# Performance work log

Hardware: AMD Instinct MI355X
Metric: run time of the kernel (lower is better)

Reference implementation:

```python
import jax, jax.numpy as jnp
import numpy as np

B, S, D, H = 4, 2048, 768, 12
DK = D // H

def setup_inputs() -> dict:
    key = jax.random.key(0)
    ks = jax.random.split(key, 9)
    s = 0.02
    return {
        "z": jax.random.normal(ks[0], (B, S, D), dtype=jnp.float32),
        "wq_w": jax.random.normal(ks[1], (D, D), dtype=jnp.float32) * s,
        "wq_b": jnp.zeros((D,), dtype=jnp.float32),
        "wk_w": jax.random.normal(ks[2], (D, D), dtype=jnp.float32) * s,
        "wk_b": jnp.zeros((D,), dtype=jnp.float32),
        "wv_w": jax.random.normal(ks[3], (D, D), dtype=jnp.float32) * s,
        "wv_b": jnp.zeros((D,), dtype=jnp.float32),
        "fc_w": jax.random.normal(ks[4], (D, D), dtype=jnp.float32) * s,
        "fc_b": jnp.zeros((D,), dtype=jnp.float32),
    }

def reference(z, wq_w, wq_b, wk_w, wk_b, wv_w, wv_b, fc_w, fc_b):
    # Dropout layers are treated as eval-mode (identity), as is standard for
    # a deterministic correctness baseline.
    b, s, d = z.shape
    temp = jnp.asarray(DK ** 0.5, dtype=z.dtype)
    # QKV projections -> [b, h, s, dk]
    def proj(w, bias):
        return (z @ w.T + bias).reshape(b, s, H, DK).transpose(0, 2, 1, 3)
    q = proj(wq_w, wq_b)
    k = proj(wk_w, wk_b)
    v = proj(wv_w, wv_b)
    # raw attention weights (pre-softmax), as returned by ScaleDotAttention
    attn_weights = jnp.einsum('bhqd,bhkd->bhqk', q / temp, k)  # [b,h,s,s]
    attn_probs = jax.nn.softmax(attn_weights, axis=-1)
    context = jnp.einsum('bhqk,bhkd->bhqd', attn_probs, v)  # [b,h,s,dk]
    avg_weights = jnp.sum(attn_weights, axis=1) / H  # [b,s,s]
    context = context.transpose(0, 2, 1, 3).reshape(b, s, d)
    attn_output = context @ fc_w.T + fc_b
    return attn_output, avg_weights
```

## Files before the change

### kernel.cpp

```cpp
#include <hip/hip_runtime.h>
#include <hip/hip_fp16.h>

#define Bc 4
#define Sc 2048
#define Dc 768
#define Hc 12
#define DKc 64

typedef _Float16 f16;
typedef __attribute__((ext_vector_type(8))) _Float16 f16x8;
typedef __attribute__((ext_vector_type(4))) _Float16 f16x4;
typedef __attribute__((ext_vector_type(4))) float f32x4;

static __device__ __forceinline__ f32x4 mfma16(f16x8 a, f16x8 b, f32x4 c) {
  return __builtin_amdgcn_mfma_f32_16x16x32_f16(a, b, c, 0, 0, 0);
}

#define GLD16(g, l)                                              \
  __builtin_amdgcn_global_load_lds(                              \
      (const __attribute__((address_space(1))) void*)(g),        \
      (__attribute__((address_space(3))) void*)(l), 16, 0, 0)

#define SWZ(row, colB) (((row) << 7) + ((colB) ^ (((row) & 7) << 4)))

__global__ __launch_bounds__(256) void cvt5(
    const float* __restrict__ z, const float* __restrict__ w0,
    const float* __restrict__ w1, const float* __restrict__ w2,
    const float* __restrict__ w3, f16* __restrict__ oz, f16* __restrict__ o0,
    f16* __restrict__ o1, f16* __restrict__ o2, f16* __restrict__ o3) {
  const int bid = blockIdx.x;
  const float* in;
  f16* out;
  int i0;
  if (bid < 6144)      { in = z;  out = oz; i0 = bid * 256; }
  else if (bid < 6720) { in = w0; out = o0; i0 = (bid - 6144) * 256; }
  else if (bid < 7296) { in = w1; out = o1; i0 = (bid - 6720) * 256; }
  else if (bid < 7872) { in = w2; out = o2; i0 = (bid - 7296) * 256; }
  else                 { in = w3; out = o3; i0 = (bid - 7872) * 256; }
  const int i = i0 + threadIdx.x;
  float4 v = reinterpret_cast<const float4*>(in)[i];
  f16x4 o;
  o[0] = (f16)v.x; o[1] = (f16)v.y; o[2] = (f16)v.z; o[3] = (f16)v.w;
  reinterpret_cast<f16x4*>(out)[i] = o;
}

#define GEMM_CORE(Ab, Bb, K)                                                   \
  __shared__ f16 As[128][32];                                                  \
  __shared__ f16 Bs[128][32];                                                  \
  f32x4 acc[4][4] = {};                                                        \
  const int srow = lane >> 2;                                                  \
  const int scol = (lane & 3) * 8;                                             \
  const f16* Ag = (Ab) + (long)(w * 32 + srow) * (K) + scol;                   \
  const f16* Bg = (Bb) + (long)(w * 32 + srow) * (K) + scol;                   \
  f16* As0 = &As[w * 32][0];                                                   \
  f16* As1 = &As[w * 32 + 16][0];                                              \
  f16* Bs0 = &Bs[w * 32][0];                                                   \
  f16* Bs1 = &Bs[w * 32 + 16][0];                                              \
  const long k16 = (long)16 * (K);                                             \
  for (int k0 = 0; k0 < (K); k0 += 32) {                                       \
    GLD16(Ag + k0, As0);                                                       \
    GLD16(Ag + k0 + k16, As1);                                                 \
    GLD16(Bg + k0, Bs0);                                                       \
    GLD16(Bg + k0 + k16, Bs1);                                                 \
    __syncthreads();                                                           \
    f16x8 af[4], bf[4];                                                        \
    _Pragma("unroll") for (int i = 0; i < 4; ++i) {                            \
      af[i] = *reinterpret_cast<const f16x8*>(&As[wr * 64 + i * 16 + l15][lg * 8]); \
      bf[i] = *reinterpret_cast<const f16x8*>(&Bs[wc * 64 + i * 16 + l15][lg * 8]); \
    }                                                                          \
    _Pragma("unroll") for (int mi = 0; mi < 4; ++mi)                           \
      _Pragma("unroll") for (int ni = 0; ni < 4; ++ni)                         \
        acc[mi][ni] = mfma16(af[mi], bf[ni], acc[mi][ni]);                     \
    __syncthreads();                                                           \
  }

__global__ __launch_bounds__(256) void gemm_qkv(
    const f16* __restrict__ zb, const f16* __restrict__ wq,
    const f16* __restrict__ wk, const f16* __restrict__ wv,
    const float* __restrict__ bq, const float* __restrict__ bk,
    const float* __restrict__ bv, f16* __restrict__ Qb, f16* __restrict__ Kb,
    f16* __restrict__ Vt) {
  const int tid = threadIdx.x;
  const int lane = tid & 63;
  const int w = tid >> 6;
  const int wr = w >> 1, wc = w & 1;
  const int l15 = lane & 15, lg = lane >> 4;
  const int sel = blockIdx.y / 6;
  const long m0 = (long)blockIdx.x * 128;
  const long n0 = (long)(blockIdx.y % 6) * 128;
  const f16* Bw = sel == 0 ? wq : sel == 1 ? wk : wv;
  const float* bias = sel == 0 ? bq : sel == 1 ? bk : bv;
  const f16* Ab = zb + m0 * Dc;
  const f16* Bb = Bw + n0 * Dc;

  GEMM_CORE(Ab, Bb, Dc)

  f16* dq = sel == 0 ? Qb : Kb;
#pragma unroll
  for (int mi = 0; mi < 4; ++mi) {
#pragma unroll
    for (int ni = 0; ni < 4; ++ni) {
      const long col = n0 + wc * 64 + ni * 16 + l15;
      const float bv2 = bias[col];
#pragma unroll
      for (int j = 0; j < 4; ++j) {
        const long row = m0 + wr * 64 + mi * 16 + lg * 4 + j;
        const float val = acc[mi][ni][j] + bv2;
        if (sel < 2) {
          dq[row * Dc + col] = (f16)val;
        } else {
          const long b = row >> 11, s = row & 2047;
          Vt[(b * Dc + col) * (long)Sc + s] = (f16)val;
        }
      }
    }
  }
}

template <int MODE>
__global__ __launch_bounds__(256) void gemm128(
    const f16* __restrict__ A, const f16* __restrict__ Bw,
    const float* __restrict__ bias, float* __restrict__ dst,
    int N, int K, long sAz, long sBz, long sDz, float scale) {
  const int tid = threadIdx.x;
  const int lane = tid & 63;
  const int w = tid >> 6;
  const int wr = w >> 1, wc = w & 1;
  const int l15 = lane & 15, lg = lane >> 4;
  const long m0 = (long)blockIdx.x * 128;
  const long n0 = (long)blockIdx.y * 128;
  const f16* Ab = A + (long)blockIdx.z * sAz + m0 * K;
  const f16* Bb = Bw + (long)blockIdx.z * sBz + n0 * K;

  GEMM_CORE(Ab, Bb, K)

  float* dp = dst + (long)blockIdx.z * sDz;
#pragma unroll
  for (int mi = 0; mi < 4; ++mi) {
#pragma unroll
    for (int ni = 0; ni < 4; ++ni) {
      const long col = n0 + wc * 64 + ni * 16 + l15;
      const float bv = (MODE == 3) ? 0.0f : bias[col];
#pragma unroll
      for (int j = 0; j < 4; ++j) {
        const long row = m0 + wr * 64 + mi * 16 + lg * 4 + j;
        const float val = acc[mi][ni][j] + bv;
        dp[row * N + col] = (MODE == 3) ? val * scale : val;
      }
    }
  }
}

__global__ __launch_bounds__(512) void attn8(const f16* __restrict__ Q,
                                             const f16* __restrict__ Km,
                                             const f16* __restrict__ Vt,
                                             f16* __restrict__ ctx) {
  const int tid = threadIdx.x;
  const int lane = tid & 63;
  const int w = tid >> 6;
  const int l15 = lane & 15, lg = lane >> 4;
  const int lid = (blockIdx.x & 7) * 96 + (blockIdx.x >> 3);
  const int qt = lid & 15;
  const int h  = (lid >> 4) % Hc;
  const int b  = lid / (16 * Hc);
  const int q0 = qt * 128 + w * 16;

  __shared__ f16 Ks[64 * 64];
  __shared__ f16 Vs[64 * 64];
  __shared__ f16 Ps[8 * 16 * 64];
  char* kb = (char*)Ks;
  char* vb = (char*)Vs;
  char* pb = (char*)Ps + (w << 11);

  f16x8 qf[2];
  {
    const f16* qp = Q + ((long)(b * Sc + q0 + l15)) * Dc + h * DKc + lg * 8;
    qf[0] = *reinterpret_cast<const f16x8*>(qp);
    qf[1] = *reinterpret_cast<const f16x8*>(qp + 32);
  }

  const int srow = tid >> 3;
  const int scolB = (tid & 7) * 16;
  const f16* Kg = Km + (long)(b * Sc) * Dc + h * DKc;
  const f16* Vg = Vt + ((long)(b * Dc + h * DKc)) * Sc;

  const float c2 = 0.18033688011f;
  float m2 = -1e30f, l_run = 0.f;
  f32x4 o[4] = {};

  *reinterpret_cast<f16x8*>(kb + SWZ(srow, scolB)) =
      *reinterpret_cast<const f16x8*>(Kg + (long)srow * Dc + scolB / 2);
  *reinterpret_cast<f16x8*>(vb + SWZ(srow, scolB)) =
      *reinterpret_cast<const f16x8*>(Vg + (long)srow * Sc + scolB / 2);
  __syncthreads();

  for (int kv0 = 0; kv0 < Sc; kv0 += 64) {
    const bool pf = (kv0 + 64) < Sc;
    f16x8 kr, vr;
    if (pf) {
      kr = *reinterpret_cast<const f16x8*>(Kg + (long)(kv0 + 64 + srow) * Dc + scolB / 2);
      vr = *reinterpret_cast<const f16x8*>(Vg + (long)srow * Sc + kv0 + 64 + scolB / 2);
    }

    f32x4 sc[4];
    __builtin_amdgcn_s_setprio(1);
#pragma unroll
    for (int t = 0; t < 4; ++t) {
      const int row = t * 16 + l15;
      f32x4 s = {};
      s = mfma16(*reinterpret_cast<const f16x8*>(kb + SWZ(row, lg * 16)), qf[0], s);
      s = mfma16(*reinterpret_cast<const f16x8*>(kb + SWZ(row, 64 + lg * 16)), qf[1], s);
      sc[t] = s;
    }
    __builtin_amdgcn_s_setprio(0);

    float mx = sc[0][0];
#pragma unroll
    for (int t = 0; t < 4; ++t)
#pragma unroll
      for (int j = 0; j < 4; ++j) mx = fmaxf(mx, sc[t][j]);
    const float mx2 = mx * c2;
    float al = 1.0f;
    if (!__all(mx2 <= m2 + 11.544f)) {
      float g = fmaxf(mx2, __shfl_xor(mx2, 16));
      g = fmaxf(g, __shfl_xor(g, 32));
      const float mn2 = fmaxf(m2, g);
      al = __builtin_amdgcn_exp2f(m2 - mn2);
      m2 = mn2;
#pragma unroll
      for (int c = 0; c < 4; ++c)
#pragma unroll
        for (int j = 0; j < 4; ++j) o[c][j] *= al;
    }
    float ps = 0.f;
    f16x4 pp[4];
#pragma unroll
    for (int t = 0; t < 4; ++t)
#pragma unroll
      for (int j = 0; j < 4; ++j) {
        float p = __builtin_amdgcn_exp2f(__builtin_fmaf(sc[t][j], c2, -m2));
        pp[t][j] = (f16)p;
        ps += p;
      }
    ps += __shfl_xor(ps, 16);
    ps += __shfl_xor(ps, 32);
    l_run = l_run * al + ps;

#pragma unroll
    for (int t = 0; t < 4; ++t)
      *reinterpret_cast<f16x4*>(pb + SWZ(l15, t * 32 + lg * 8)) = pp[t];
    asm volatile("s_waitcnt lgkmcnt(0)" ::: "memory");
    __builtin_amdgcn_sched_barrier(0);

    f16x8 pa0 = *reinterpret_cast<const f16x8*>(pb + SWZ(l15, lg * 16));
    f16x8 pa1 = *reinterpret_cast<const f16x8*>(pb + SWZ(l15, 64 + lg * 16));
    __builtin_amdgcn_s_setprio(1);
#pragma unroll
    for (int c = 0; c < 4; ++c) {
      const int row = c * 16 + l15;
      o[c] = mfma16(*reinterpret_cast<const f16x8*>(vb + SWZ(row, lg * 16)), pa0, o[c]);
      o[c] = mfma16(*reinterpret_cast<const f16x8*>(vb + SWZ(row, 64 + lg * 16)), pa1, o[c]);
    }
    __builtin_amdgcn_s_setprio(0);

    if (pf) {
      __syncthreads();
      *reinterpret_cast<f16x8*>(kb + SWZ(srow, scolB)) = kr;
      *reinterpret_cast<f16x8*>(vb + SWZ(srow, scolB)) = vr;
      __syncthreads();
    }
  }

  const float inv = 1.0f / l_run;
  f16* cp = ctx + ((long)(b * Sc) + q0 + l15) * Dc + h * DKc;
#pragma unroll
  for (int c = 0; c < 4; ++c) {
    f16x4 ov;
#pragma unroll
    for (int j = 0; j < 4; ++j) ov[j] = (f16)(o[c][j] * inv);
    *reinterpret_cast<f16x4*>(cp + c * 16 + lg * 4) = ov;
  }
}

extern "C" void kernel_launch(void* const* d_in, const int* in_sizes, int n_in,
                              void* d_out, int out_size, void* d_ws, size_t ws_size,
                              hipStream_t stream) {
  (void)in_sizes; (void)n_in; (void)out_size; (void)ws_size;
  const float* z    = (const float*)d_in[0];
  const float* wq_w = (const float*)d_in[1];
  const float* wq_b = (const float*)d_in[2];
  const float* wk_w = (const float*)d_in[3];
  const float* wk_b = (const float*)d_in[4];
  const float* wv_w = (const float*)d_in[5];
  const float* wv_b = (const float*)d_in[6];
  const float* fc_w = (const float*)d_in[7];
  const float* fc_b = (const float*)d_in[8];
  float* out = (float*)d_out;

  char* ws = (char*)d_ws;
  size_t off = 0;
  auto alloc = [&](size_t bytes) -> void* {
    void* p = (void*)(ws + off);
    off += (bytes + 255) & ~(size_t)255;
    return p;
  };
  const size_t zdb = (size_t)Bc * Sc * Dc * sizeof(f16);
  const size_t wdb = (size_t)Dc * Dc * sizeof(f16);
  f16* zb  = (f16*)alloc(zdb);
  f16* wqb = (f16*)alloc(wdb);
  f16* wkb = (f16*)alloc(wdb);
  f16* wvb = (f16*)alloc(wdb);
  f16* fcb = (f16*)alloc(wdb);
  f16* Qb  = (f16*)alloc(zdb);
  f16* Kb  = (f16*)alloc(zdb);
  f16* Vt  = (f16*)alloc(zdb);
  f16* Cx  = zb;

  cvt5<<<8448, 256, 0, stream>>>(z, wq_w, wk_w, wv_w, fc_w, zb, wqb, wkb, wvb, fcb);

  dim3 gqkv(Bc * Sc / 128, 18, 1);
  gemm_qkv<<<gqkv, 256, 0, stream>>>(zb, wqb, wkb, wvb, wq_b, wk_b, wv_b, Qb, Kb, Vt);

  dim3 gavg(Sc / 128, Sc / 128, Bc);
  gemm128<3><<<gavg, 256, 0, stream>>>(Qb, Kb, nullptr, out + (size_t)Bc * Sc * Dc,
                                       Sc, Dc, (long)Sc * Dc, (long)Sc * Dc,
                                       (long)Sc * Sc, 1.0f / 96.0f);

  attn8<<<Bc * Hc * (Sc / 128), 512, 0, stream>>>(Qb, Kb, Vt, Cx);

  dim3 gfc(Bc * Sc / 128, Dc / 128, 1);
  gemm128<2><<<gfc, 256, 0, stream>>>(Cx, fcb, fc_b, out, Dc, Dc, 0, 0, 0, 1.f);
}
```

Measured before the change: 221.8 us.

## Fuse attention and head-averaged score GEMM into one heterogeneous launch

Merges the flash-attention kernel and the head-averaged QK^T GEMM into a single kernel. Blocks are assigned per XCD in a 3:4 ratio: three attention tiles for every four GEMM tiles. The intent is to overlap the write-heavy average-weights GEMM with the compute-heavy attention so both use the GPU at once, and to drop one launch. In exchange, the GEMM branch is a simpler single-buffered LDS loop without swizzling, which may be less efficient than the previous GEMM core. The fused kernel also fixes 32KB of shared memory and sets a launch-bounds occupancy hint.

```diff
diff --git a/kernel.cpp b/kernel.cpp
--- a/kernel.cpp
+++ b/kernel.cpp
@@ -117,11 +117,9 @@
   }
 }
 
-template <int MODE>
-__global__ __launch_bounds__(256) void gemm128(
+__global__ __launch_bounds__(256) void gemm_fc(
     const f16* __restrict__ A, const f16* __restrict__ Bw,
-    const float* __restrict__ bias, float* __restrict__ dst,
-    int N, int K, long sAz, long sBz, long sDz, float scale) {
+    const float* __restrict__ bias, float* __restrict__ dst, int N, int K) {
   const int tid = threadIdx.x;
   const int lane = tid & 63;
   const int w = tid >> 6;
@@ -129,156 +127,209 @@
   const int l15 = lane & 15, lg = lane >> 4;
   const long m0 = (long)blockIdx.x * 128;
   const long n0 = (long)blockIdx.y * 128;
-  const f16* Ab = A + (long)blockIdx.z * sAz + m0 * K;
-  const f16* Bb = Bw + (long)blockIdx.z * sBz + n0 * K;
+  const f16* Ab = A + m0 * K;
+  const f16* Bb = Bw + n0 * K;
 
   GEMM_CORE(Ab, Bb, K)
 
-  float* dp = dst + (long)blockIdx.z * sDz;
 #pragma unroll
   for (int mi = 0; mi < 4; ++mi) {
 #pragma unroll
     for (int ni = 0; ni < 4; ++ni) {
       const long col = n0 + wc * 64 + ni * 16 + l15;
-      const float bv = (MODE == 3) ? 0.0f : bias[col];
+      const float bv = bias[col];
 #pragma unroll
       for (int j = 0; j < 4; ++j) {
         const long row = m0 + wr * 64 + mi * 16 + lg * 4 + j;
-        const float val = acc[mi][ni][j] + bv;
-        dp[row * N + col] = (MODE == 3) ? val * scale : val;
+        dst[row * N + col] = acc[mi][ni][j] + bv;
       }
     }
   }
 }
 
-__global__ __launch_bounds__(512) void attn8(const f16* __restrict__ Q,
-                                             const f16* __restrict__ Km,
-                                             const f16* __restrict__ Vt,
-                                             f16* __restrict__ ctx) {
+__global__ __launch_bounds__(512, 4) void fused_aw(
+    const f16* __restrict__ Q, const f16* __restrict__ Km,
+    const f16* __restrict__ Vt, f16* __restrict__ ctx,
+    float* __restrict__ avg) {
+  __shared__ f16 smem[16384];
   const int tid = threadIdx.x;
   const int lane = tid & 63;
   const int w = tid >> 6;
   const int l15 = lane & 15, lg = lane >> 4;
-  const int lid = (blockIdx.x & 7) * 96 + (blockIdx.x >> 3);
-  const int qt = lid & 15;
-  const int h  = (lid >> 4) % Hc;
-  const int b  = lid / (16 * Hc);
-  const int q0 = qt * 128 + w * 16;
-
-  __shared__ f16 Ks[64 * 64];
-  __shared__ f16 Vs[64 * 64];
-  __shared__ f16 Ps[8 * 16 * 64];
-  char* kb = (char*)Ks;
-  char* vb = (char*)Vs;
-  char* pb = (char*)Ps + (w << 11);
-
-  f16x8 qf[2];
-  {
-    const f16* qp = Q + ((long)(b * Sc + q0 + l15)) * Dc + h * DKc + lg * 8;
-    qf[0] = *reinterpret_cast<const f16x8*>(qp);
-    qf[1] = *reinterpret_cast<const f16x8*>(qp + 32);
-  }
-
-  const int srow = tid >> 3;
-  const int scolB = (tid & 7) * 16;
-  const f16* Kg = Km + (long)(b * Sc) * Dc + h * DKc;
-  const f16* Vg = Vt + ((long)(b * Dc + h * DKc)) * Sc;
-
-  const float c2 = 0.18033688011f;
-  float m2 = -1e30f, l_run = 0.f;
-  f32x4 o[4] = {};
-
-  *reinterpret_cast<f16x8*>(kb + SWZ(srow, scolB)) =
-      *reinterpret_cast<const f16x8*>(Kg + (long)srow * Dc + scolB / 2);
-  *reinterpret_cast<f16x8*>(vb + SWZ(srow, scolB)) =
-      *reinterpret_cast<const f16x8*>(Vg + (long)srow * Sc + scolB / 2);
-  __syncthreads();
-
-  for (int kv0 = 0; kv0 < Sc; kv0 += 64) {
-    const bool pf = (kv0 + 64) < Sc;
-    f16x8 kr, vr;
-    if (pf) {
-      kr = *reinterpret_cast<const f16x8*>(Kg + (long)(kv0 + 64 + srow) * Dc + scolB / 2);
-      vr = *reinterpret_cast<const f16x8*>(Vg + (long)srow * Sc + kv0 + 64 + scolB / 2);
-    }
-
-    f32x4 sc[4];
-    __builtin_amdgcn_s_setprio(1);
-#pragma unroll
-    for (int t = 0; t < 4; ++t) {
-      const int row = t * 16 + l15;
-      f32x4 s = {};
-      s = mfma16(*reinterpret_cast<const f16x8*>(kb + SWZ(row, lg * 16)), qf[0], s);
-      s = mfma16(*reinterpret_cast<const f16x8*>(kb + SWZ(row, 64 + lg * 16)), qf[1], s);
-      sc[t] = s;
-    }
-    __builtin_amdgcn_s_setprio(0);
-
-    float mx = sc[0][0];
-#pragma unroll
-    for (int t = 0; t < 4; ++t)
-#pragma unroll
-      for (int j = 0; j < 4; ++j) mx = fmaxf(mx, sc[t][j]);
-    const float mx2 = mx * c2;
-    float al = 1.0f;
-    if (!__all(mx2 <= m2 + 11.544f)) {
-      float g = fmaxf(mx2, __shfl_xor(mx2, 16));
-      g = fmaxf(g, __shfl_xor(g, 32));
-      const float mn2 = fmaxf(m2, g);
-      al = __builtin_amdgcn_exp2f(m2 - mn2);
-      m2 = mn2;
-#pragma unroll
-      for (int c = 0; c < 4; ++c)
-#pragma unroll
-        for (int j = 0; j < 4; ++j) o[c][j] *= al;
-    }
-    float ps = 0.f;
-    f16x4 pp[4];
-#pragma unroll
-    for (int t = 0; t < 4; ++t)
-#pragma unroll
-      for (int j = 0; j < 4; ++j) {
-        float p = __builtin_amdgcn_exp2f(__builtin_fmaf(sc[t][j], c2, -m2));
-        pp[t][j] = (f16)p;
-        ps += p;
-      }
-    ps += __shfl_xor(ps, 16);
-    ps += __shfl_xor(ps, 32);
-    l_run = l_run * al + ps;
-
-#pragma unroll
-    for (int t = 0; t < 4; ++t)
-      *reinterpret_cast<f16x4*>(pb + SWZ(l15, t * 32 + lg * 8)) = pp[t];
-    asm volatile("s_waitcnt lgkmcnt(0)" ::: "memory");
-    __builtin_amdgcn_sched_barrier(0);
-
-    f16x8 pa0 = *reinterpret_cast<const f16x8*>(pb + SWZ(l15, lg * 16));
-    f16x8 pa1 = *reinterpret_cast<const f16x8*>(pb + SWZ(l15, 64 + lg * 16));
-    __builtin_amdgcn_s_setprio(1);
+  const int bid = blockIdx.x;
+  const int xcd = bid & 7, slot = bid >> 3;
+  const int g = slot / 7, r = slot - g * 7;
+
+  if (r < 3) {
+    const int lid = xcd * 96 + g * 3 + r;
+    const int qt = lid & 15;
+    const int h  = (lid >> 4) % Hc;
+    const int b  = lid / (16 * Hc);
+    const int q0 = qt * 128 + w * 16;
+
+    char* kb = (char*)smem;
+    char* vb = (char*)smem + 8192;
+    char* pb = (char*)smem + 16384 + (w << 11);
+
+    f16x8 qf[2];
+    {
+      const f16* qp = Q + ((long)(b * Sc + q0 + l15)) * Dc + h * DKc + lg * 8;
+      qf[0] = *reinterpret_cast<const f16x8*>(qp);
+      qf[1] = *reinterpret_cast<const f16x8*>(qp + 32);
+    }
+
+    const int srow = tid >> 3;
+    const int scolB = (tid & 7) * 16;
+    const f16* Kg = Km + (long)(b * Sc) * Dc + h * DKc;
+    const f16* Vg = Vt + ((long)(b * Dc + h * DKc)) * Sc;
+
+    const float c2 = 0.18033688011f;
+    float m2 = -1e30f, l_run = 0.f;
+    f32x4 o[4] = {};
+
+    *reinterpret_cast<f16x8*>(kb + SWZ(srow, scolB)) =
+        *reinterpret_cast<const f16x8*>(Kg + (long)srow * Dc + scolB / 2);
+    *reinterpret_cast<f16x8*>(vb + SWZ(srow, scolB)) =
+        *reinterpret_cast<const f16x8*>(Vg + (long)srow * Sc + scolB / 2);
+    __syncthreads();
+
+    for (int kv0 = 0; kv0 < Sc; kv0 += 64) {
+      const bool pf = (kv0 + 64) < Sc;
+      f16x8 kr, vr;
+      if (pf) {
+        kr = *reinterpret_cast<const f16x8*>(Kg + (long)(kv0 + 64 + srow) * Dc + scolB / 2);
+        vr = *reinterpret_cast<const f16x8*>(Vg + (long)srow * Sc + kv0 + 64 + scolB / 2);
+      }
+
+      f32x4 sc[4];
+      __builtin_amdgcn_s_setprio(1);
+#pragma unroll
+      for (int t = 0; t < 4; ++t) {
+        const int row = t * 16 + l15;
+        f32x4 s = {};
+        s = mfma16(*reinterpret_cast<const f16x8*>(kb + SWZ(row, lg * 16)), qf[0], s);
+        s = mfma16(*reinterpret_cast<const f16x8*>(kb + SWZ(row, 64 + lg * 16)), qf[1], s);
+        sc[t] = s;
+      }
+      __builtin_amdgcn_s_setprio(0);
+
+      float mx = sc[0][0];
+#pragma unroll
+      for (int t = 0; t < 4; ++t)
+#pragma unroll
+        for (int j = 0; j < 4; ++j) mx = fmaxf(mx, sc[t][j]);
+      const float mx2 = mx * c2;
+      float al = 1.0f;
+      if (!__all(mx2 <= m2 + 11.544f)) {
+        float gm = fmaxf(mx2, __shfl_xor(mx2, 16));
+        gm = fmaxf(gm, __shfl_xor(gm, 32));
+        const float mn2 = fmaxf(m2, gm);
+        al = __builtin_amdgcn_exp2f(m2 - mn2);
+        m2 = mn2;
+#pragma unroll
+        for (int c = 0; c < 4; ++c)
+#pragma unroll
+          for (int j = 0; j < 4; ++j) o[c][j] *= al;
+      }
+      float ps = 0.f;
+      f16x4 pp[4];
+#pragma unroll
+      for (int t = 0; t < 4; ++t)
+#pragma unroll
+        for (int j = 0; j < 4; ++j) {
+          float p = __builtin_amdgcn_exp2f(__builtin_fmaf(sc[t][j], c2, -m2));
+          pp[t][j] = (f16)p;
+          ps += p;
+        }
+      ps += __shfl_xor(ps, 16);
+      ps += __shfl_xor(ps, 32);
+      l_run = l_run * al + ps;
+
+#pragma unroll
+      for (int t = 0; t < 4; ++t)
+        *reinterpret_cast<f16x4*>(pb + SWZ(l15, t * 32 + lg * 8)) = pp[t];
+      asm volatile("s_waitcnt lgkmcnt(0)" ::: "memory");
+      __builtin_amdgcn_sched_barrier(0);
+
+      f16x8 pa0 = *reinterpret_cast<const f16x8*>(pb + SWZ(l15, lg * 16));
+      f16x8 pa1 = *reinterpret_cast<const f16x8*>(pb + SWZ(l15, 64 + lg * 16));
+      __builtin_amdgcn_s_setprio(1);
+#pragma unroll
+      for (int c = 0; c < 4; ++c) {
+        const int row = c * 16 + l15;
+        o[c] = mfma16(*reinterpret_cast<const f16x8*>(vb + SWZ(row, lg * 16)), pa0, o[c]);
+        o[c] = mfma16(*reinterpret_cast<const f16x8*>(vb + SWZ(row, 64 + lg * 16)), pa1, o[c]);
+      }
+      __builtin_amdgcn_s_setprio(0);
+
+      if (pf) {
+        __syncthreads();
+        *reinterpret_cast<f16x8*>(kb + SWZ(srow, scolB)) = kr;
+        *reinterpret_cast<f16x8*>(vb + SWZ(srow, scolB)) = vr;
+        __syncthreads();
+      }
+    }
+
+    const float inv = 1.0f / l_run;
+    f16* cp = ctx + ((long)(b * Sc) + q0 + l15) * Dc + h * DKc;
 #pragma unroll
     for (int c = 0; c < 4; ++c) {
-      const int row = c * 16 + l15;
-      o[c] = mfma16(*reinterpret_cast<const f16x8*>(vb + SWZ(row, lg * 16)), pa0, o[c]);
-      o[c] = mfma16(*reinterpret_cast<const f16x8*>(vb + SWZ(row, 64 + lg * 16)), pa1, o[c]);
-    }
-    __builtin_amdgcn_s_setprio(0);
-
-    if (pf) {
+      f16x4 ov;
+#pragma unroll
+      for (int j = 0; j < 4; ++j) ov[j] = (f16)(o[c][j] * inv);
+      *reinterpret_cast<f16x4*>(cp + c * 16 + lg * 4) = ov;
+    }
+  } else {
+    const int chunk = xcd * 128 + g * 4 + (r - 3);
+    const int b  = chunk >> 8;
+    const int t  = chunk & 255;
+    const long m0 = (long)(t >> 4) * 128;
+    const long n0 = (long)(t & 15) * 128;
+    const int wr = w >> 2, wc = w & 3;
+
+    f16* As = smem;
+    f16* Bs = smem + 4096;
+    const f16* Ab = Q + (long)b * Sc * Dc + m0 * Dc;
+    const f16* Bb = Km + (long)b * Sc * Dc + n0 * Dc;
+    const f16* Ag = Ab + (long)(tid >> 2) * Dc + (tid & 3) * 8;
+    const f16* Bg = Bb + (long)(tid >> 2) * Dc + (tid & 3) * 8;
+    f16* AsD = As + w * 512;
+    f16* BsD = Bs + w * 512;
+
+    f32x4 acc[4][2] = {};
+
+    for (int k0 = 0; k0 < Dc; k0 += 32) {
+      GLD16(Ag + k0, AsD);
+      GLD16(Bg + k0, BsD);
       __syncthreads();
-      *reinterpret_cast<f16x8*>(kb + SWZ(srow, scolB)) = kr;
-      *reinterpret_cast<f16x8*>(vb + SWZ(srow, scolB)) = vr;
+      f16x8 af[4], bf[2];
+#pragma unroll
+      for (int i = 0; i < 4; ++i)
+        af[i] = *reinterpret_cast<const f16x8*>(&As[(wr * 64 + i * 16 + l15) * 32 + lg * 8]);
+#pragma unroll
+      for (int n = 0; n < 2; ++n)
+        bf[n] = *reinterpret_cast<const f16x8*>(&Bs[(wc * 32 + n * 16 + l15) * 32 + lg * 8]);
+#pragma unroll
+      for (int mi = 0; mi < 4; ++mi)
+#pragma unroll
+        for (int ni = 0; ni < 2; ++ni)
+          acc[mi][ni] = mfma16(af[mi], bf[ni], acc[mi][ni]);
       __syncthreads();
     }
-  }
-
-  const float inv = 1.0f / l_run;
-  f16* cp = ctx + ((long)(b * Sc) + q0 + l15) * Dc + h * DKc;
-#pragma unroll
-  for (int c = 0; c < 4; ++c) {
-    f16x4 ov;
-#pragma unroll
-    for (int j = 0; j < 4; ++j) ov[j] = (f16)(o[c][j] * inv);
-    *reinterpret_cast<f16x4*>(cp + c * 16 + lg * 4) = ov;
+
+    float* dp = avg + (long)b * Sc * Sc;
+#pragma unroll
+    for (int mi = 0; mi < 4; ++mi) {
+#pragma unroll
+      for (int ni = 0; ni < 2; ++ni) {
+        const long col = n0 + wc * 32 + ni * 16 + l15;
+#pragma unroll
+        for (int j = 0; j < 4; ++j) {
+          const long row = m0 + wr * 64 + mi * 16 + lg * 4 + j;
+          dp[row * Sc + col] = acc[mi][ni][j] * (1.0f / 96.0f);
+        }
+      }
+    }
   }
 }
 
@@ -321,13 +372,8 @@
   dim3 gqkv(Bc * Sc / 128, 18, 1);
   gemm_qkv<<<gqkv, 256, 0, stream>>>(zb, wqb, wkb, wvb, wq_b, wk_b, wv_b, Qb, Kb, Vt);
 
-  dim3 gavg(Sc / 128, Sc / 128, Bc);
-  gemm128<3><<<gavg, 256, 0, stream>>>(Qb, Kb, nullptr, out + (size_t)Bc * Sc * Dc,
-                                       Sc, Dc, (long)Sc * Dc, (long)Sc * Dc,
-                                       (long)Sc * Sc, 1.0f / 96.0f);
-
-  attn8<<<Bc * Hc * (Sc / 128), 512, 0, stream>>>(Qb, Kb, Vt, Cx);
+  fused_aw<<<1792, 512, 0, stream>>>(Qb, Kb, Vt, Cx, out + (size_t)Bc * Sc * Dc);
 
   dim3 gfc(Bc * Sc / 128, Dc / 128, 1);
-  gemm128<2><<<gfc, 256, 0, stream>>>(Cx, fcb, fc_b, out, Dc, Dc, 0, 0, 0, 1.f);
-}
+  gemm_fc<<<gfc, 256, 0, stream>>>(Cx, fcb, fc_b, out, Dc, Dc);
+}
```

New measurement: 227.5 us. +2.6%, slower.

## Use double-buffered 256x256 GEMM tiles for QKV and averaged-score kernels

Applied to the files above, without the earlier changes.

Replaces the 128x128 single-buffered QKV projection and averaged attention-score GEMMs with a new 256x256-tile, 512-thread kernel. The new kernel double-buffers LDS loads via global_load_lds with explicit vmcnt waits, and remaps block IDs so neighbouring tiles land on the same XCD. The larger tiles raise operand reuse and the prefetch overlaps global loads with MFMA work. In exchange each block uses more registers and LDS, the grids shrink to 288 and 256 blocks (fewer waves to spread across CUs), and the LDS reads use no swizzle, so bank conflicts are possible.

```diff
diff --git a/kernel.cpp b/kernel.cpp
--- a/kernel.cpp
+++ b/kernel.cpp
@@ -42,6 +42,156 @@
   f16x4 o;
   o[0] = (f16)v.x; o[1] = (f16)v.y; o[2] = (f16)v.z; o[3] = (f16)v.w;
   reinterpret_cast<f16x4*>(out)[i] = o;
+}
+
+template <int MODE>
+__global__ __launch_bounds__(512, 2) void gemm256x(
+    const f16* __restrict__ A0, const f16* __restrict__ W0,
+    const f16* __restrict__ W1, const f16* __restrict__ W2,
+    const float* __restrict__ bq, const float* __restrict__ bk,
+    const float* __restrict__ bv, f16* __restrict__ Qb, f16* __restrict__ Kb,
+    f16* __restrict__ Vt, float* __restrict__ avg) {
+  constexpr int K = Dc;
+  constexpr int NK = K / 32;
+  const int tid = threadIdx.x;
+  const int lane = tid & 63;
+  const int w = tid >> 6;
+  const int wr = w >> 2, wc = w & 3;
+  const int l15 = lane & 15, lg = lane >> 4;
+
+  const f16* Ab;
+  const f16* Bb;
+  long m0;
+  int seg = 0, n0seg = 0, bat = 0, ncol0 = 0;
+  if (MODE == 0) {
+    const int wgid = (blockIdx.x & 7) * 36 + (blockIdx.x >> 3);
+    const int mx = wgid / 9, nt = wgid % 9;
+    m0 = (long)mx * 256;
+    seg = nt / 3;
+    n0seg = (nt % 3) * 256;
+    const f16* Wsel = seg == 0 ? W0 : seg == 1 ? W1 : W2;
+    Ab = A0 + m0 * K;
+    Bb = Wsel + (long)n0seg * K;
+  } else {
+    const int wgid = (blockIdx.x & 7) * 32 + (blockIdx.x >> 3);
+    bat = wgid >> 6;
+    const int t = wgid & 63;
+    const int mx = t >> 3, nx = t & 7;
+    m0 = (long)mx * 256;
+    ncol0 = nx * 256;
+    Ab = W0 + (long)bat * Sc * Dc + m0 * K;
+    Bb = W1 + (long)bat * Sc * Dc + (long)ncol0 * K;
+  }
+
+  __shared__ f16 AB[2][2][256 * 32];
+
+  const int strow = (w * 2) * 16 + (lane >> 2);
+  const int stcol = (lane & 3) * 8;
+  const f16* Ag0 = Ab + (long)strow * K + stcol;
+  const f16* Ag1 = Ag0 + (long)16 * K;
+  const f16* Bg0 = Bb + (long)strow * K + stcol;
+  const f16* Bg1 = Bg0 + (long)16 * K;
+  const int so0 = w * 1024;
+  const int so1 = w * 1024 + 512;
+
+#define STG(buf, k0)                          \
+  {                                           \
+    GLD16(Ag0 + (k0), &AB[buf][0][so0]);      \
+    GLD16(Ag1 + (k0), &AB[buf][0][so1]);      \
+    GLD16(Bg0 + (k0), &AB[buf][1][so0]);      \
+    GLD16(Bg1 + (k0), &AB[buf][1][so1]);      \
+  }
+
+  f32x4 acc[8][4] = {};
+
+  STG(0, 0)
+  STG(1, 32)
+
+#pragma unroll 1
+  for (int i = 0; i < NK; ++i) {
+    if (i + 1 < NK) {
+      asm volatile("s_waitcnt vmcnt(4)" ::: "memory");
+    } else {
+      asm volatile("s_waitcnt vmcnt(0)" ::: "memory");
+    }
+    __builtin_amdgcn_sched_barrier(0);
+    __builtin_amdgcn_s_barrier();
+    __builtin_amdgcn_sched_barrier(0);
+
+    const f16* Asb = &AB[i & 1][0][0];
+    const f16* Bsb = &AB[i & 1][1][0];
+    f16x8 af[8], bf[4];
+#pragma unroll
+    for (int mi = 0; mi < 8; ++mi)
+      af[mi] = *reinterpret_cast<const f16x8*>(
+          &Asb[(wr * 128 + mi * 16 + l15) * 32 + lg * 8]);
+#pragma unroll
+    for (int ni = 0; ni < 4; ++ni)
+      bf[ni] = *reinterpret_cast<const f16x8*>(
+          &Bsb[(wc * 64 + ni * 16 + l15) * 32 + lg * 8]);
+#pragma unroll
+    for (int mi = 0; mi < 8; ++mi)
+#pragma unroll
+      for (int ni = 0; ni < 4; ++ni)
+        acc[mi][ni] = mfma16(af[mi], bf[ni], acc[mi][ni]);
+
+    __builtin_amdgcn_sched_barrier(0);
+    __builtin_amdgcn_s_barrier();
+    __builtin_amdgcn_sched_barrier(0);
+    if (i + 2 < NK) STG(i & 1, (i + 2) * 32)
+  }
+#undef STG
+
+  if (MODE == 0) {
+    const float* bias = seg == 0 ? bq : seg == 1 ? bk : bv;
+    float bvv[4];
+#pragma unroll
+    for (int ni = 0; ni < 4; ++ni)
+      bvv[ni] = bias[n0seg + wc * 64 + ni * 16 + l15];
+    if (seg < 2) {
+      f16* dq = seg == 0 ? Qb : Kb;
+#pragma unroll
+      for (int mi = 0; mi < 8; ++mi) {
+#pragma unroll
+        for (int ni = 0; ni < 4; ++ni) {
+          const long col = n0seg + wc * 64 + ni * 16 + l15;
+#pragma unroll
+          for (int j = 0; j < 4; ++j) {
+            const long row = m0 + wr * 128 + mi * 16 + lg * 4 + j;
+            dq[row * Dc + col] = (f16)(acc[mi][ni][j] + bvv[ni]);
+          }
+        }
+      }
+    } else {
+#pragma unroll
+      for (int mi = 0; mi < 8; ++mi) {
+#pragma unroll
+        for (int ni = 0; ni < 4; ++ni) {
+          const long col = n0seg + wc * 64 + ni * 16 + l15;
+#pragma unroll
+          for (int j = 0; j < 4; ++j) {
+            const long row = m0 + wr * 128 + mi * 16 + lg * 4 + j;
+            const long b = row >> 11, s = row & 2047;
+            Vt[(b * Dc + col) * (long)Sc + s] = (f16)(acc[mi][ni][j] + bvv[ni]);
+          }
+        }
+      }
+    }
+  } else {
+    float* dp = avg + (long)bat * Sc * Sc;
+#pragma unroll
+    for (int mi = 0; mi < 8; ++mi) {
+#pragma unroll
+      for (int ni = 0; ni < 4; ++ni) {
+        const long col = ncol0 + wc * 64 + ni * 16 + l15;
+#pragma unroll
+        for (int j = 0; j < 4; ++j) {
+          const long row = m0 + wr * 128 + mi * 16 + lg * 4 + j;
+          dp[row * Sc + col] = acc[mi][ni][j] * (1.0f / 96.0f);
+        }
+      }
+    }
+  }
 }
 
 #define GEMM_CORE(Ab, Bb, K)                                                   \
@@ -74,54 +224,9 @@
     __syncthreads();                                                           \
   }
 
-__global__ __launch_bounds__(256) void gemm_qkv(
-    const f16* __restrict__ zb, const f16* __restrict__ wq,
-    const f16* __restrict__ wk, const f16* __restrict__ wv,
-    const float* __restrict__ bq, const float* __restrict__ bk,
-    const float* __restrict__ bv, f16* __restrict__ Qb, f16* __restrict__ Kb,
-    f16* __restrict__ Vt) {
-  const int tid = threadIdx.x;
-  const int lane = tid & 63;
-  const int w = tid >> 6;
-  const int wr = w >> 1, wc = w & 1;
-  const int l15 = lane & 15, lg = lane >> 4;
-  const int sel = blockIdx.y / 6;
-  const long m0 = (long)blockIdx.x * 128;
-  const long n0 = (long)(blockIdx.y % 6) * 128;
-  const f16* Bw = sel == 0 ? wq : sel == 1 ? wk : wv;
-  const float* bias = sel == 0 ? bq : sel == 1 ? bk : bv;
-  const f16* Ab = zb + m0 * Dc;
-  const f16* Bb = Bw + n0 * Dc;
-
-  GEMM_CORE(Ab, Bb, Dc)
-
-  f16* dq = sel == 0 ? Qb : Kb;
-#pragma unroll
-  for (int mi = 0; mi < 4; ++mi) {
-#pragma unroll
-    for (int ni = 0; ni < 4; ++ni) {
-      const long col = n0 + wc * 64 + ni * 16 + l15;
-      const float bv2 = bias[col];
-#pragma unroll
-      for (int j = 0; j < 4; ++j) {
-        const long row = m0 + wr * 64 + mi * 16 + lg * 4 + j;
-        const float val = acc[mi][ni][j] + bv2;
-        if (sel < 2) {
-          dq[row * Dc + col] = (f16)val;
-        } else {
-          const long b = row >> 11, s = row & 2047;
-          Vt[(b * Dc + col) * (long)Sc + s] = (f16)val;
-        }
-      }
-    }
-  }
-}
-
-template <int MODE>
-__global__ __launch_bounds__(256) void gemm128(
+__global__ __launch_bounds__(256) void gemm_fc(
     const f16* __restrict__ A, const f16* __restrict__ Bw,
-    const float* __restrict__ bias, float* __restrict__ dst,
-    int N, int K, long sAz, long sBz, long sDz, float scale) {
+    const float* __restrict__ bias, float* __restrict__ dst, int N, int K) {
   const int tid = threadIdx.x;
   const int lane = tid & 63;
   const int w = tid >> 6;
@@ -129,23 +234,21 @@
   const int l15 = lane & 15, lg = lane >> 4;
   const long m0 = (long)blockIdx.x * 128;
   const long n0 = (long)blockIdx.y * 128;
-  const f16* Ab = A + (long)blockIdx.z * sAz + m0 * K;
-  const f16* Bb = Bw + (long)blockIdx.z * sBz + n0 * K;
+  const f16* Ab = A + m0 * K;
+  const f16* Bb = Bw + n0 * K;
 
   GEMM_CORE(Ab, Bb, K)
 
-  float* dp = dst + (long)blockIdx.z * sDz;
 #pragma unroll
   for (int mi = 0; mi < 4; ++mi) {
 #pragma unroll
     for (int ni = 0; ni < 4; ++ni) {
       const long col = n0 + wc * 64 + ni * 16 + l15;
-      const float bv = (MODE == 3) ? 0.0f : bias[col];
+      const float bv = bias[col];
 #pragma unroll
       for (int j = 0; j < 4; ++j) {
         const long row = m0 + wr * 64 + mi * 16 + lg * 4 + j;
-        const float val = acc[mi][ni][j] + bv;
-        dp[row * N + col] = (MODE == 3) ? val * scale : val;
+        dst[row * N + col] = acc[mi][ni][j] + bv;
       }
     }
   }
@@ -318,16 +421,15 @@
 
   cvt5<<<8448, 256, 0, stream>>>(z, wq_w, wk_w, wv_w, fc_w, zb, wqb, wkb, wvb, fcb);
 
-  dim3 gqkv(Bc * Sc / 128, 18, 1);
-  gemm_qkv<<<gqkv, 256, 0, stream>>>(zb, wqb, wkb, wvb, wq_b, wk_b, wv_b, Qb, Kb, Vt);
-
-  dim3 gavg(Sc / 128, Sc / 128, Bc);
-  gemm128<3><<<gavg, 256, 0, stream>>>(Qb, Kb, nullptr, out + (size_t)Bc * Sc * Dc,
-                                       Sc, Dc, (long)Sc * Dc, (long)Sc * Dc,
-                                       (long)Sc * Sc, 1.0f / 96.0f);
+  gemm256x<0><<<288, 512, 0, stream>>>(zb, wqb, wkb, wvb, wq_b, wk_b, wv_b,
+                                       Qb, Kb, Vt, nullptr);
+
+  gemm256x<1><<<256, 512, 0, stream>>>(nullptr, Qb, Kb, nullptr, nullptr,
+                                       nullptr, nullptr, nullptr, nullptr,
+                                       nullptr, out + (size_t)Bc * Sc * Dc);
 
   attn8<<<Bc * Hc * (Sc / 128), 512, 0, stream>>>(Qb, Kb, Vt, Cx);
 
   dim3 gfc(Bc * Sc / 128, Dc / 128, 1);
-  gemm128<2><<<gfc, 256, 0, stream>>>(Cx, fcb, fc_b, out, Dc, Dc, 0, 0, 0, 1.f);
-}
+  gemm_fc<<<gfc, 256, 0, stream>>>(Cx, fcb, fc_b, out, Dc, Dc);
+}
```

After: 204.9 us. -7.6%, faster.
